# Optimization experiments

Measured on AMD Instinct MI355X. Metric: run time of the kernel, lower is better.

## Reference

```python
import jax, jax.numpy as jnp
import numpy as np

SCALING = 32.0 / 16.0  # alpha / r

def setup_inputs() -> dict:
    key = jax.random.key(0)
    k1, k2, k3, k4 = jax.random.split(key, 4)
    B_, S, D_in, D_out, R = 4, 2048, 4096, 4096, 16
    x = jax.random.normal(k1, (B_, S, D_in), dtype=jnp.float32)
    W_base = jax.random.normal(k2, (D_out, D_in), dtype=jnp.float32) * 0.02
    b_base = jax.random.normal(k3, (D_out,), dtype=jnp.float32) * 0.02
    A = jax.random.normal(k4, (R, D_in), dtype=jnp.float32) * 0.02
    B = jnp.zeros((D_out, R), dtype=jnp.float32)  # lora_B init to zeros
    return {"x": x, "W_base": W_base, "b_base": b_base, "A": A, "B": B}

def reference(x, W_base, b_base, A, B):
    # base linear (stands in for dequantized 4-bit matmul): [B,S,Din] @ [Din,Dout]
    out = jnp.einsum('bsd,od->bso', x, W_base) + b_base
    # LoRA path: B(A(x)) * scaling, dropout=0 -> identity
    xa = jnp.einsum('bsd,rd->bsr', x, A)        # [B,S,r]
    delta = jnp.einsum('bsr,or->bso', xa, B)    # [B,S,Dout]
    return out + delta * SCALING
```

## Files before the change

### kernel.cpp

```cpp
#include <hip/hip_runtime.h>


typedef __attribute__((ext_vector_type(4))) float f32x4;
typedef __attribute__((ext_vector_type(8))) short bf16x8;

__device__ __forceinline__ unsigned short f2bf(float f) {
    unsigned u = __builtin_bit_cast(unsigned, f);
    unsigned r = u + 0x7fffu + ((u >> 16) & 1u);
    return (unsigned short)(r >> 16);
}

__device__ __forceinline__ void gload_lds16(const void* g, void* l) {
    __builtin_amdgcn_global_load_lds(
        (const __attribute__((address_space(1))) void*)g,
        (__attribute__((address_space(3))) void*)l, 16, 0, 0);
}

__global__ __launch_bounds__(256) void cast_x_kernel(
    const float* __restrict__ x, unsigned short* __restrict__ xb, int n8)
{
    int stride = gridDim.x * blockDim.x;
    for (int i = blockIdx.x * blockDim.x + threadIdx.x; i < n8; i += stride) {
        size_t base = (size_t)i * 8;
        float4 f0 = *(const float4*)&x[base];
        float4 f1 = *(const float4*)&x[base + 4];
        ushort4 o0, o1;
        o0.x = f2bf(f0.x); o0.y = f2bf(f0.y); o0.z = f2bf(f0.z); o0.w = f2bf(f0.w);
        o1.x = f2bf(f1.x); o1.y = f2bf(f1.y); o1.z = f2bf(f1.z); o1.w = f2bf(f1.w);
        *(ushort4*)&xb[base]     = o0;
        *(ushort4*)&xb[base + 4] = o1;
    }
}

__global__ __launch_bounds__(256) void prep_w_kernel(
    const float* __restrict__ W, const float* __restrict__ A,
    const float* __restrict__ Bl, unsigned short* __restrict__ wb,
    int K, float scale)
{
    __shared__ float Bs[16][16];
    const int t = threadIdx.x;
    const int n0 = blockIdx.y * 16;
    const int k0 = blockIdx.x * 256;
    {
        int nl = t >> 4, r = t & 15;
        Bs[nl][r] = Bl[(size_t)(n0 + nl) * 16 + r];
    }
    __syncthreads();

    const int lane = t & 63;
    const int wv = t >> 6;
    const int k = k0 + lane * 4;

    float4 av[16];
#pragma unroll
    for (int r = 0; r < 16; ++r)
        av[r] = *(const float4*)&A[(size_t)r * K + k];

#pragma unroll
    for (int j = 0; j < 4; ++j) {
        const int nl = wv * 4 + j;
        const int n = n0 + nl;
        float4 w = *(const float4*)&W[(size_t)n * K + k];
        float d0 = 0.f, d1 = 0.f, d2 = 0.f, d3 = 0.f;
#pragma unroll
        for (int r = 0; r < 16; ++r) {
            float b = Bs[nl][r];
            d0 += b * av[r].x; d1 += b * av[r].y;
            d2 += b * av[r].z; d3 += b * av[r].w;
        }
        ushort4 o;
        o.x = f2bf(w.x + scale * d0);
        o.y = f2bf(w.y + scale * d1);
        o.z = f2bf(w.z + scale * d2);
        o.w = f2bf(w.w + scale * d3);
        *(ushort4*)&wb[(size_t)n * K + k] = o;
    }
}


#define BARRIER()  __builtin_amdgcn_s_barrier()

__global__ __launch_bounds__(512, 2) void gemm256_kernel(
    const unsigned short* __restrict__ Xb, const unsigned short* __restrict__ Wb,
    const float* __restrict__ bias, float* __restrict__ out,
    int M, int N, int K)
{
    __shared__ __align__(16) unsigned short lds[2][2][2][8192];

    const int NT = K / 64;
    const int ntn = N / 256;
    int bid = blockIdx.x;
    {
        int per = gridDim.x >> 3;
        bid = (bid & 7) * per + (bid >> 3);
    }
    const int tm = bid / ntn, tn = bid % ntn;

    const int t = threadIdx.x;
    const int lane = t & 63, wave = t >> 6;
    const int wr = wave >> 2;
    const int wc = wave & 3;

    const int srow = t >> 3;
    const int scol = ((t & 7) * 8) ^ (((t >> 3) & 7) << 3);
    unsigned gA[2][2], gB[2][2];
#pragma unroll
    for (int h = 0; h < 2; ++h)
#pragma unroll
        for (int i = 0; i < 2; ++i) {
            gA[h][i] = (unsigned)((tm * 256 + h * 128 + i * 64 + srow) * K + scol);
            gB[h][i] = (unsigned)((tn * 256 + h * 128 + i * 64 + srow) * K + scol);
        }

#define STAGE_A(buf, kt)                                                        \
    _Pragma("unroll") for (int h = 0; h < 2; ++h)                               \
    _Pragma("unroll") for (int i = 0; i < 2; ++i)                               \
        gload_lds16(Xb + gA[h][i] + (kt) * 64,                                  \
                    &lds[buf][0][h][i * 4096 + wave * 512]);
#define STAGE_B(buf, kt)                                                        \
    _Pragma("unroll") for (int h = 0; h < 2; ++h)                               \
    _Pragma("unroll") for (int i = 0; i < 2; ++i)                               \
        gload_lds16(Wb + gB[h][i] + (kt) * 64,                                  \
                    &lds[buf][1][h][i * 4096 + wave * 512]);

    const int fr = lane & 15;
    const int hi16 = ((lane >> 4) & 3) * 16;
    const int bsw = (fr & 7) << 4;
    const int lo0 = hi16 ^ bsw;
    const int lo1 = (64 + hi16) ^ bsw;

    f32x4 acc[8][4] = {};

    STAGE_A(0, 0); STAGE_B(0, 0);
    STAGE_A(1, 1); STAGE_B(1, 1);
    asm volatile("s_waitcnt vmcnt(8)" ::: "memory");
    BARRIER();

    for (int kt = 0; kt < NT; ++kt) {
        const int cur = kt & 1;
        const char* pA = (const char*)&lds[cur][0][wr][0];
        const char* pB = (const char*)&lds[cur][1][wc >> 1][0];
        const int bro = (wc & 1) * 64;

        bf16x8 a[8][2], b[4][2];
#pragma unroll
        for (int mi = 0; mi < 8; ++mi) {
            a[mi][0] = *(const bf16x8*)(pA + (mi * 16 + fr) * 128 + lo0);
            a[mi][1] = *(const bf16x8*)(pA + (mi * 16 + fr) * 128 + lo1);
        }
#pragma unroll
        for (int ni = 0; ni < 4; ++ni) {
            b[ni][0] = *(const bf16x8*)(pB + (bro + ni * 16 + fr) * 128 + lo0);
            b[ni][1] = *(const bf16x8*)(pB + (bro + ni * 16 + fr) * 128 + lo1);
        }

#pragma unroll
        for (int kk = 0; kk < 2; ++kk)
#pragma unroll
            for (int mi = 0; mi < 8; ++mi)
#pragma unroll
                for (int ni = 0; ni < 4; ++ni)
                    acc[mi][ni] = __builtin_amdgcn_mfma_f32_16x16x32_bf16(
                        a[mi][kk], b[ni][kk], acc[mi][ni], 0, 0, 0);

        asm volatile("s_waitcnt lgkmcnt(0)" ::: "memory");
        BARRIER();
        if (kt + 2 < NT) {
            STAGE_A(cur, kt + 2); STAGE_B(cur, kt + 2);
            asm volatile("s_waitcnt vmcnt(8)" ::: "memory");
        } else {
            asm volatile("s_waitcnt vmcnt(0)" ::: "memory");
        }
        BARRIER();
    }

    const int row0 = tm * 256 + wr * 128 + (lane >> 4) * 4;
    const int col0 = tn * 256 + wc * 64;
#pragma unroll
    for (int ni = 0; ni < 4; ++ni) {
        const int col = col0 + ni * 16 + fr;
        const float bv = bias[col];
#pragma unroll
        for (int mi = 0; mi < 8; ++mi) {
            const int row = row0 + mi * 16;
#pragma unroll
            for (int r = 0; r < 4; ++r)
                out[(size_t)(row + r) * N + col] = acc[mi][ni][r] + bv;
        }
    }
}

extern "C" void kernel_launch(void* const* d_in, const int* in_sizes, int n_in,
                              void* d_out, int out_size, void* d_ws, size_t ws_size,
                              hipStream_t stream)
{
    const float* x  = (const float*)d_in[0];
    const float* W  = (const float*)d_in[1];
    const float* b  = (const float*)d_in[2];
    const float* A  = (const float*)d_in[3];
    const float* Bl = (const float*)d_in[4];
    float* out = (float*)d_out;

    const int Dout = in_sizes[2];
    const int Din  = in_sizes[1] / Dout;
    const int M    = in_sizes[0] / Din;

    unsigned short* xb = (unsigned short*)d_ws;
    unsigned short* wb = xb + (size_t)M * Din;

    cast_x_kernel<<<2048, 256, 0, stream>>>(x, xb, M * Din / 8);

    dim3 gw(Din / 256, Dout / 16);
    prep_w_kernel<<<gw, 256, 0, stream>>>(W, A, Bl, wb, Din, 2.0f);

    const int grid = (M / 256) * (Dout / 256);
    gemm256_kernel<<<grid, 512, 0, stream>>>(xb, wb, b, out, M, Dout, Din);
}
```

Measured before the change: 322.3 us.

## Use 4 waves with 128x128 per-wave tiles and interleave staging with MFMA halves

Result: slower. 351.5 us (+9.1%).

```diff
diff --git a/kernel.cpp b/kernel.cpp
--- a/kernel.cpp
+++ b/kernel.cpp
@@ -79,8 +79,9 @@
 
 
 #define BARRIER()  __builtin_amdgcn_s_barrier()
-
-__global__ __launch_bounds__(512, 2) void gemm256_kernel(
+#define LGKM0()    asm volatile("s_waitcnt lgkmcnt(0)" ::: "memory")
+
+__global__ __launch_bounds__(256, 1) void gemm256_kernel(
     const unsigned short* __restrict__ Xb, const unsigned short* __restrict__ Wb,
     const float* __restrict__ bias, float* __restrict__ out,
     int M, int N, int K)
@@ -98,8 +99,8 @@
 
     const int t = threadIdx.x;
     const int lane = t & 63, wave = t >> 6;
-    const int wr = wave >> 2;
-    const int wc = wave & 3;
+    const int wr = wave >> 1;
+    const int wc = wave & 1;
 
     const int srow = t >> 3;
     const int scol = ((t & 7) * 8) ^ (((t >> 3) & 7) << 3);
@@ -111,17 +112,22 @@
             gA[h][i] = (unsigned)((tm * 256 + h * 128 + i * 64 + srow) * K + scol);
             gB[h][i] = (unsigned)((tn * 256 + h * 128 + i * 64 + srow) * K + scol);
         }
-
-#define STAGE_A(buf, kt)                                                        \
-    _Pragma("unroll") for (int h = 0; h < 2; ++h)                               \
-    _Pragma("unroll") for (int i = 0; i < 2; ++i)                               \
-        gload_lds16(Xb + gA[h][i] + (kt) * 64,                                  \
-                    &lds[buf][0][h][i * 4096 + wave * 512]);
-#define STAGE_B(buf, kt)                                                        \
-    _Pragma("unroll") for (int h = 0; h < 2; ++h)                               \
-    _Pragma("unroll") for (int i = 0; i < 2; ++i)                               \
-        gload_lds16(Wb + gB[h][i] + (kt) * 64,                                  \
-                    &lds[buf][1][h][i * 4096 + wave * 512]);
+    const unsigned jstep = 32u * (unsigned)K;
+
+#define ST_A(buf, h, ktt)                                                       \
+    _Pragma("unroll") for (int i = 0; i < 2; ++i) {                             \
+        gload_lds16(Xb + gA[h][i] + (ktt) * 64,                                 \
+                    &lds[buf][0][h][i * 4096 + wave * 512]);                    \
+        gload_lds16(Xb + gA[h][i] + jstep + (ktt) * 64,                         \
+                    &lds[buf][0][h][i * 4096 + 2048 + wave * 512]);             \
+    }
+#define ST_B(buf, h, ktt)                                                       \
+    _Pragma("unroll") for (int i = 0; i < 2; ++i) {                             \
+        gload_lds16(Wb + gB[h][i] + (ktt) * 64,                                 \
+                    &lds[buf][1][h][i * 4096 + wave * 512]);                    \
+        gload_lds16(Wb + gB[h][i] + jstep + (ktt) * 64,                         \
+                    &lds[buf][1][h][i * 4096 + 2048 + wave * 512]);             \
+    }
 
     const int fr = lane & 15;
     const int hi16 = ((lane >> 4) & 3) * 16;
@@ -129,44 +135,56 @@
     const int lo0 = hi16 ^ bsw;
     const int lo1 = (64 + hi16) ^ bsw;
 
-    f32x4 acc[8][4] = {};
-
-    STAGE_A(0, 0); STAGE_B(0, 0);
-    STAGE_A(1, 1); STAGE_B(1, 1);
+    f32x4 acc[8][8] = {};
+
+#pragma unroll
+    for (int h = 0; h < 2; ++h) { ST_A(0, h, 0) ST_B(0, h, 0) }
+#pragma unroll
+    for (int h = 0; h < 2; ++h) { ST_A(1, h, 1) }
     asm volatile("s_waitcnt vmcnt(8)" ::: "memory");
     BARRIER();
 
     for (int kt = 0; kt < NT; ++kt) {
         const int cur = kt & 1;
         const char* pA = (const char*)&lds[cur][0][wr][0];
-        const char* pB = (const char*)&lds[cur][1][wc >> 1][0];
-        const int bro = (wc & 1) * 64;
-
-        bf16x8 a[8][2], b[4][2];
-#pragma unroll
-        for (int mi = 0; mi < 8; ++mi) {
-            a[mi][0] = *(const bf16x8*)(pA + (mi * 16 + fr) * 128 + lo0);
-            a[mi][1] = *(const bf16x8*)(pA + (mi * 16 + fr) * 128 + lo1);
-        }
-#pragma unroll
-        for (int ni = 0; ni < 4; ++ni) {
-            b[ni][0] = *(const bf16x8*)(pB + (bro + ni * 16 + fr) * 128 + lo0);
-            b[ni][1] = *(const bf16x8*)(pB + (bro + ni * 16 + fr) * 128 + lo1);
-        }
-
-#pragma unroll
-        for (int kk = 0; kk < 2; ++kk)
-#pragma unroll
-            for (int mi = 0; mi < 8; ++mi)
-#pragma unroll
-                for (int ni = 0; ni < 4; ++ni)
-                    acc[mi][ni] = __builtin_amdgcn_mfma_f32_16x16x32_bf16(
-                        a[mi][kk], b[ni][kk], acc[mi][ni], 0, 0, 0);
-
-        asm volatile("s_waitcnt lgkmcnt(0)" ::: "memory");
+        const char* pB = (const char*)&lds[cur][1][wc][0];
+        const bool stB = (kt + 1 < NT);
+        const bool stA = (kt + 2 < NT);
+
+        bf16x8 a0[8], b0[8], a1[8], b1[8];
+
+#pragma unroll
+        for (int i = 0; i < 8; ++i) {
+            a0[i] = *(const bf16x8*)(pA + (i * 16 + fr) * 128 + lo0);
+            b0[i] = *(const bf16x8*)(pB + (i * 16 + fr) * 128 + lo0);
+        }
+#pragma unroll
+        for (int mi = 0; mi < 8; ++mi)
+#pragma unroll
+            for (int ni = 0; ni < 8; ++ni)
+                acc[mi][ni] = __builtin_amdgcn_mfma_f32_16x16x32_bf16(
+                    a0[mi], b0[ni], acc[mi][ni], 0, 0, 0);
+
+#pragma unroll
+        for (int i = 0; i < 8; ++i) {
+            a1[i] = *(const bf16x8*)(pA + (i * 16 + fr) * 128 + lo1);
+            b1[i] = *(const bf16x8*)(pB + (i * 16 + fr) * 128 + lo1);
+        }
+
+        LGKM0();
         BARRIER();
-        if (kt + 2 < NT) {
-            STAGE_A(cur, kt + 2); STAGE_B(cur, kt + 2);
+
+        if (stB) { ST_B(cur ^ 1, 0, kt + 1) ST_B(cur ^ 1, 1, kt + 1) }
+        if (stA) { ST_A(cur, 0, kt + 2) ST_A(cur, 1, kt + 2) }
+
+#pragma unroll
+        for (int mi = 0; mi < 8; ++mi)
+#pragma unroll
+            for (int ni = 0; ni < 8; ++ni)
+                acc[mi][ni] = __builtin_amdgcn_mfma_f32_16x16x32_bf16(
+                    a1[mi], b1[ni], acc[mi][ni], 0, 0, 0);
+
+        if (stA) {
             asm volatile("s_waitcnt vmcnt(8)" ::: "memory");
         } else {
             asm volatile("s_waitcnt vmcnt(0)" ::: "memory");
@@ -175,9 +193,9 @@
     }
 
     const int row0 = tm * 256 + wr * 128 + (lane >> 4) * 4;
-    const int col0 = tn * 256 + wc * 64;
-#pragma unroll
-    for (int ni = 0; ni < 4; ++ni) {
+    const int col0 = tn * 256 + wc * 128;
+#pragma unroll
+    for (int ni = 0; ni < 8; ++ni) {
         const int col = col0 + ni * 16 + fr;
         const float bv = bias[col];
 #pragma unroll
@@ -214,5 +232,5 @@
     prep_w_kernel<<<gw, 256, 0, stream>>>(W, A, Bl, wb, Din, 2.0f);
 
     const int grid = (M / 256) * (Dout / 256);
-    gemm256_kernel<<<grid, 512, 0, stream>>>(xb, wb, b, out, M, Dout, Din);
-}
+    gemm256_kernel<<<grid, 256, 0, stream>>>(xb, wb, b, out, M, Dout, Din);
+}
```

## Switch to 128x128 GEMM tile with interleaved LDS loads, staging and MFMA phases

Applied to the files above, without the earlier changes.

Result: slower. 380.2 us (+18.0%).

```diff
diff --git a/kernel.cpp b/kernel.cpp
--- a/kernel.cpp
+++ b/kernel.cpp
@@ -78,17 +78,20 @@
 }
 
 
+#define SETPRIO(p) __builtin_amdgcn_s_setprio(p)
 #define BARRIER()  __builtin_amdgcn_s_barrier()
-
-__global__ __launch_bounds__(512, 2) void gemm256_kernel(
+#define LGKM0()    do { asm volatile("s_waitcnt lgkmcnt(0)" ::: "memory"); \
+                        __builtin_amdgcn_sched_barrier(0); } while (0)
+
+__global__ __launch_bounds__(256, 2) void gemm128_kernel(
     const unsigned short* __restrict__ Xb, const unsigned short* __restrict__ Wb,
     const float* __restrict__ bias, float* __restrict__ out,
     int M, int N, int K)
 {
-    __shared__ __align__(16) unsigned short lds[2][2][2][8192];
+    __shared__ __align__(16) unsigned short lds[2][2][8192];
 
     const int NT = K / 64;
-    const int ntn = N / 256;
+    const int ntn = N / 128;
     int bid = blockIdx.x;
     {
         int per = gridDim.x >> 3;
@@ -98,30 +101,23 @@
 
     const int t = threadIdx.x;
     const int lane = t & 63, wave = t >> 6;
-    const int wr = wave >> 2;
-    const int wc = wave & 3;
+    const int wr = wave >> 1;
+    const int wc = wave & 1;
 
     const int srow = t >> 3;
     const int scol = ((t & 7) * 8) ^ (((t >> 3) & 7) << 3);
-    unsigned gA[2][2], gB[2][2];
-#pragma unroll
-    for (int h = 0; h < 2; ++h)
-#pragma unroll
-        for (int i = 0; i < 2; ++i) {
-            gA[h][i] = (unsigned)((tm * 256 + h * 128 + i * 64 + srow) * K + scol);
-            gB[h][i] = (unsigned)((tn * 256 + h * 128 + i * 64 + srow) * K + scol);
-        }
-
-#define STAGE_A(buf, kt)                                                        \
-    _Pragma("unroll") for (int h = 0; h < 2; ++h)                               \
-    _Pragma("unroll") for (int i = 0; i < 2; ++i)                               \
-        gload_lds16(Xb + gA[h][i] + (kt) * 64,                                  \
-                    &lds[buf][0][h][i * 4096 + wave * 512]);
-#define STAGE_B(buf, kt)                                                        \
-    _Pragma("unroll") for (int h = 0; h < 2; ++h)                               \
-    _Pragma("unroll") for (int i = 0; i < 2; ++i)                               \
-        gload_lds16(Wb + gB[h][i] + (kt) * 64,                                  \
-                    &lds[buf][1][h][i * 4096 + wave * 512]);
+    const unsigned gA0 = (unsigned)((tm * 128 + srow) * K + scol);
+    const unsigned gB0 = (unsigned)((tn * 128 + srow) * K + scol);
+    const unsigned jstep = 32u * (unsigned)K;
+
+#define ST_A(buf, ktt)                                                          \
+    _Pragma("unroll") for (int j = 0; j < 4; ++j)                               \
+        gload_lds16(Xb + gA0 + j * jstep + (ktt) * 64,                          \
+                    &lds[buf][0][j * 2048 + wave * 512]);
+#define ST_B(buf, ktt)                                                          \
+    _Pragma("unroll") for (int j = 0; j < 4; ++j)                               \
+        gload_lds16(Wb + gB0 + j * jstep + (ktt) * 64,                          \
+                    &lds[buf][1][j * 2048 + wave * 512]);
 
     const int fr = lane & 15;
     const int hi16 = ((lane >> 4) & 3) * 16;
@@ -129,44 +125,68 @@
     const int lo0 = hi16 ^ bsw;
     const int lo1 = (64 + hi16) ^ bsw;
 
-    f32x4 acc[8][4] = {};
-
-    STAGE_A(0, 0); STAGE_B(0, 0);
-    STAGE_A(1, 1); STAGE_B(1, 1);
+    f32x4 acc[4][4] = {};
+
+    ST_A(0, 0) ST_B(0, 0)
+    ST_A(1, 1) ST_B(1, 1)
     asm volatile("s_waitcnt vmcnt(8)" ::: "memory");
     BARRIER();
 
+#define MFMA_N2(n0)                                                             \
+    _Pragma("unroll") for (int mi = 0; mi < 4; ++mi)                            \
+    _Pragma("unroll") for (int ni = n0; ni < n0 + 2; ++ni)                      \
+    _Pragma("unroll") for (int kk = 0; kk < 2; ++kk)                            \
+        acc[mi][ni] = __builtin_amdgcn_mfma_f32_16x16x32_bf16(                  \
+            a[mi][kk], b[ni][kk], acc[mi][ni], 0, 0, 0);
+#define MFMA_N1(n0)                                                             \
+    _Pragma("unroll") for (int mi = 0; mi < 4; ++mi)                            \
+    _Pragma("unroll") for (int kk = 0; kk < 2; ++kk)                            \
+        acc[mi][n0] = __builtin_amdgcn_mfma_f32_16x16x32_bf16(                  \
+            a[mi][kk], b[n0][kk], acc[mi][n0], 0, 0, 0);
+
     for (int kt = 0; kt < NT; ++kt) {
         const int cur = kt & 1;
-        const char* pA = (const char*)&lds[cur][0][wr][0];
-        const char* pB = (const char*)&lds[cur][1][wc >> 1][0];
-        const int bro = (wc & 1) * 64;
-
-        bf16x8 a[8][2], b[4][2];
-#pragma unroll
-        for (int mi = 0; mi < 8; ++mi) {
-            a[mi][0] = *(const bf16x8*)(pA + (mi * 16 + fr) * 128 + lo0);
-            a[mi][1] = *(const bf16x8*)(pA + (mi * 16 + fr) * 128 + lo1);
-        }
-#pragma unroll
-        for (int ni = 0; ni < 4; ++ni) {
-            b[ni][0] = *(const bf16x8*)(pB + (bro + ni * 16 + fr) * 128 + lo0);
-            b[ni][1] = *(const bf16x8*)(pB + (bro + ni * 16 + fr) * 128 + lo1);
-        }
-
-#pragma unroll
-        for (int kk = 0; kk < 2; ++kk)
-#pragma unroll
-            for (int mi = 0; mi < 8; ++mi)
-#pragma unroll
-                for (int ni = 0; ni < 4; ++ni)
-                    acc[mi][ni] = __builtin_amdgcn_mfma_f32_16x16x32_bf16(
-                        a[mi][kk], b[ni][kk], acc[mi][ni], 0, 0, 0);
-
-        asm volatile("s_waitcnt lgkmcnt(0)" ::: "memory");
-        BARRIER();
-        if (kt + 2 < NT) {
-            STAGE_A(cur, kt + 2); STAGE_B(cur, kt + 2);
+        const char* pA = (const char*)&lds[cur][0][0];
+        const char* pB = (const char*)&lds[cur][1][0];
+        const bool st = (kt + 2 < NT);
+
+        bf16x8 a[4][2], b[4][2];
+
+#pragma unroll
+        for (int mi = 0; mi < 4; ++mi) {
+            a[mi][0] = *(const bf16x8*)(pA + (wr * 64 + mi * 16 + fr) * 128 + lo0);
+            a[mi][1] = *(const bf16x8*)(pA + (wr * 64 + mi * 16 + fr) * 128 + lo1);
+        }
+#pragma unroll
+        for (int ni = 0; ni < 2; ++ni) {
+            b[ni][0] = *(const bf16x8*)(pB + (wc * 64 + ni * 16 + fr) * 128 + lo0);
+            b[ni][1] = *(const bf16x8*)(pB + (wc * 64 + ni * 16 + fr) * 128 + lo1);
+        }
+        BARRIER();
+        LGKM0();
+        SETPRIO(1);
+        MFMA_N2(0)
+        SETPRIO(0);
+        BARRIER();
+
+#pragma unroll
+        for (int ni = 2; ni < 4; ++ni) {
+            b[ni][0] = *(const bf16x8*)(pB + (wc * 64 + ni * 16 + fr) * 128 + lo0);
+            b[ni][1] = *(const bf16x8*)(pB + (wc * 64 + ni * 16 + fr) * 128 + lo1);
+        }
+        if (st) { ST_A(cur, kt + 2) }
+        BARRIER();
+        LGKM0();
+        SETPRIO(1);
+        MFMA_N1(2)
+        SETPRIO(0);
+        BARRIER();
+
+        if (st) { ST_B(cur, kt + 2) }
+        SETPRIO(1);
+        MFMA_N1(3)
+        SETPRIO(0);
+        if (st) {
             asm volatile("s_waitcnt vmcnt(8)" ::: "memory");
         } else {
             asm volatile("s_waitcnt vmcnt(0)" ::: "memory");
@@ -174,14 +194,14 @@
         BARRIER();
     }
 
-    const int row0 = tm * 256 + wr * 128 + (lane >> 4) * 4;
-    const int col0 = tn * 256 + wc * 64;
+    const int row0 = tm * 128 + wr * 64 + (lane >> 4) * 4;
+    const int col0 = tn * 128 + wc * 64;
 #pragma unroll
     for (int ni = 0; ni < 4; ++ni) {
         const int col = col0 + ni * 16 + fr;
         const float bv = bias[col];
 #pragma unroll
-        for (int mi = 0; mi < 8; ++mi) {
+        for (int mi = 0; mi < 4; ++mi) {
             const int row = row0 + mi * 16;
 #pragma unroll
             for (int r = 0; r < 4; ++r)
@@ -213,6 +233,6 @@
     dim3 gw(Din / 256, Dout / 16);
     prep_w_kernel<<<gw, 256, 0, stream>>>(W, A, Bl, wb, Din, 2.0f);
 
-    const int grid = (M / 256) * (Dout / 256);
-    gemm256_kernel<<<grid, 512, 0, stream>>>(xb, wb, b, out, M, Dout, Din);
-}
+    const int grid = (M / 128) * (Dout / 128);
+    gemm128_kernel<<<grid, 256, 0, stream>>>(xb, wb, b, out, M, Dout, Din);
+}
```

## Interleave LDS fragment loads with quartered MFMA blocks and prefetch next tile

Applied to the files above, without the earlier changes.

New measurement: 301.7 us. 1.07x faster.

```diff
diff --git a/kernel.cpp b/kernel.cpp
--- a/kernel.cpp
+++ b/kernel.cpp
@@ -78,7 +78,9 @@
 }
 
 
+#define SETPRIO(p) __builtin_amdgcn_s_setprio(p)
 #define BARRIER()  __builtin_amdgcn_s_barrier()
+#define LGKM0()    asm volatile("s_waitcnt lgkmcnt(0)" ::: "memory")
 
 __global__ __launch_bounds__(512, 2) void gemm256_kernel(
     const unsigned short* __restrict__ Xb, const unsigned short* __restrict__ Wb,
@@ -100,6 +102,8 @@
     const int lane = t & 63, wave = t >> 6;
     const int wr = wave >> 2;
     const int wc = wave & 3;
+    const int wch = wc >> 1;
+    const int bro = (wc & 1) * 64;
 
     const int srow = t >> 3;
     const int scol = ((t & 7) * 8) ^ (((t >> 3) & 7) << 3);
@@ -112,15 +116,15 @@
             gB[h][i] = (unsigned)((tn * 256 + h * 128 + i * 64 + srow) * K + scol);
         }
 
-#define STAGE_A(buf, kt)                                                        \
+#define ST_A4(buf, ktt)                                                         \
     _Pragma("unroll") for (int h = 0; h < 2; ++h)                               \
     _Pragma("unroll") for (int i = 0; i < 2; ++i)                               \
-        gload_lds16(Xb + gA[h][i] + (kt) * 64,                                  \
+        gload_lds16(Xb + gA[h][i] + (ktt) * 64,                                 \
                     &lds[buf][0][h][i * 4096 + wave * 512]);
-#define STAGE_B(buf, kt)                                                        \
+#define ST_B4(buf, ktt)                                                         \
     _Pragma("unroll") for (int h = 0; h < 2; ++h)                               \
     _Pragma("unroll") for (int i = 0; i < 2; ++i)                               \
-        gload_lds16(Wb + gB[h][i] + (kt) * 64,                                  \
+        gload_lds16(Wb + gB[h][i] + (ktt) * 64,                                 \
                     &lds[buf][1][h][i * 4096 + wave * 512]);
 
     const int fr = lane & 15;
@@ -130,47 +134,92 @@
     const int lo1 = (64 + hi16) ^ bsw;
 
     f32x4 acc[8][4] = {};
-
-    STAGE_A(0, 0); STAGE_B(0, 0);
-    STAGE_A(1, 1); STAGE_B(1, 1);
+    bf16x8 a03[4][2], a47[4][2], b01[2][2], b23[2][2];
+
+    ST_A4(0, 0) ST_B4(0, 0)
+    ST_A4(1, 1) ST_B4(1, 1)
     asm volatile("s_waitcnt vmcnt(8)" ::: "memory");
     BARRIER();
+    {
+        const char* pA = (const char*)&lds[0][0][wr][0];
+        const char* pB = (const char*)&lds[0][1][wch][0];
+#pragma unroll
+        for (int i = 0; i < 4; ++i) {
+            a03[i][0] = *(const bf16x8*)(pA + (i * 16 + fr) * 128 + lo0);
+            a03[i][1] = *(const bf16x8*)(pA + (i * 16 + fr) * 128 + lo1);
+        }
+#pragma unroll
+        for (int i = 0; i < 2; ++i) {
+            b01[i][0] = *(const bf16x8*)(pB + (bro + i * 16 + fr) * 128 + lo0);
+            b01[i][1] = *(const bf16x8*)(pB + (bro + i * 16 + fr) * 128 + lo1);
+        }
+    }
+
+#define MFMA_Q(AV, BV, M0, N0)                                                  \
+    _Pragma("unroll") for (int mi = 0; mi < 4; ++mi)                            \
+    _Pragma("unroll") for (int ni = 0; ni < 2; ++ni)                            \
+    _Pragma("unroll") for (int kk = 0; kk < 2; ++kk)                            \
+        acc[(M0) + mi][(N0) + ni] = __builtin_amdgcn_mfma_f32_16x16x32_bf16(    \
+            AV[mi][kk], BV[ni][kk], acc[(M0) + mi][(N0) + ni], 0, 0, 0);
 
     for (int kt = 0; kt < NT; ++kt) {
         const int cur = kt & 1;
-        const char* pA = (const char*)&lds[cur][0][wr][0];
-        const char* pB = (const char*)&lds[cur][1][wc >> 1][0];
-        const int bro = (wc & 1) * 64;
-
-        bf16x8 a[8][2], b[4][2];
-#pragma unroll
-        for (int mi = 0; mi < 8; ++mi) {
-            a[mi][0] = *(const bf16x8*)(pA + (mi * 16 + fr) * 128 + lo0);
-            a[mi][1] = *(const bf16x8*)(pA + (mi * 16 + fr) * 128 + lo1);
-        }
-#pragma unroll
-        for (int ni = 0; ni < 4; ++ni) {
-            b[ni][0] = *(const bf16x8*)(pB + (bro + ni * 16 + fr) * 128 + lo0);
-            b[ni][1] = *(const bf16x8*)(pB + (bro + ni * 16 + fr) * 128 + lo1);
-        }
-
-#pragma unroll
-        for (int kk = 0; kk < 2; ++kk)
-#pragma unroll
-            for (int mi = 0; mi < 8; ++mi)
-#pragma unroll
-                for (int ni = 0; ni < 4; ++ni)
-                    acc[mi][ni] = __builtin_amdgcn_mfma_f32_16x16x32_bf16(
-                        a[mi][kk], b[ni][kk], acc[mi][ni], 0, 0, 0);
-
-        asm volatile("s_waitcnt lgkmcnt(0)" ::: "memory");
-        BARRIER();
-        if (kt + 2 < NT) {
-            STAGE_A(cur, kt + 2); STAGE_B(cur, kt + 2);
-            asm volatile("s_waitcnt vmcnt(8)" ::: "memory");
-        } else {
-            asm volatile("s_waitcnt vmcnt(0)" ::: "memory");
-        }
+        const char* pA  = (const char*)&lds[cur][0][wr][0];
+        const char* pB  = (const char*)&lds[cur][1][wch][0];
+        const char* pA1 = (const char*)&lds[cur ^ 1][0][wr][0];
+        const char* pB1 = (const char*)&lds[cur ^ 1][1][wch][0];
+        const bool stB = (kt + 1 < NT);
+        const bool stA = (kt + 2 < NT);
+
+        LGKM0();
+#pragma unroll
+        for (int i = 0; i < 4; ++i) {
+            a47[i][0] = *(const bf16x8*)(pA + ((4 + i) * 16 + fr) * 128 + lo0);
+            a47[i][1] = *(const bf16x8*)(pA + ((4 + i) * 16 + fr) * 128 + lo1);
+        }
+        SETPRIO(1);
+        MFMA_Q(a03, b01, 0, 0)
+        SETPRIO(0);
+        BARRIER();
+
+        LGKM0();
+#pragma unroll
+        for (int i = 0; i < 2; ++i) {
+            b23[i][0] = *(const bf16x8*)(pB + (bro + (2 + i) * 16 + fr) * 128 + lo0);
+            b23[i][1] = *(const bf16x8*)(pB + (bro + (2 + i) * 16 + fr) * 128 + lo1);
+        }
+        SETPRIO(1);
+        MFMA_Q(a47, b01, 4, 0)
+        SETPRIO(0);
+        asm volatile("s_waitcnt vmcnt(0)" ::: "memory");
+        BARRIER();
+
+        LGKM0();
+        if (stB) {
+#pragma unroll
+            for (int i = 0; i < 2; ++i) {
+                b01[i][0] = *(const bf16x8*)(pB1 + (bro + i * 16 + fr) * 128 + lo0);
+                b01[i][1] = *(const bf16x8*)(pB1 + (bro + i * 16 + fr) * 128 + lo1);
+            }
+        }
+        if (stA) { ST_A4(cur, kt + 2) }
+        SETPRIO(1);
+        MFMA_Q(a03, b23, 0, 2)
+        SETPRIO(0);
+        BARRIER();
+
+        LGKM0();
+        if (stB) {
+#pragma unroll
+            for (int i = 0; i < 4; ++i) {
+                a03[i][0] = *(const bf16x8*)(pA1 + (i * 16 + fr) * 128 + lo0);
+                a03[i][1] = *(const bf16x8*)(pA1 + (i * 16 + fr) * 128 + lo1);
+            }
+        }
+        if (stA) { ST_B4(cur, kt + 2) }
+        SETPRIO(1);
+        MFMA_Q(a47, b23, 4, 2)
+        SETPRIO(0);
         BARRIER();
     }
 
```
